# Kernel optimization log

Hardware: AMD Instinct MI355X
Metric: run time of the kernel (lower is better)

Reference implementation:

```python
import jax, jax.numpy as jnp
import numpy as np

N0_SRC, N0_DST, E0 = 495616, 45056, 450560
N1_DST, E1 = 4096, 40960
IN_FEATS, N_HIDDEN, N_CLASSES = 256, 128, 16


def setup_inputs() -> dict:
    key = jax.random.key(0)
    ks = jax.random.split(key, 12)
    x = jax.random.normal(ks[0], (N0_SRC, IN_FEATS), dtype=jnp.float32)
    src0 = jax.random.randint(ks[1], (E0,), 0, N0_SRC, dtype=jnp.int32)
    dst0 = jax.random.randint(ks[2], (E0,), 0, N0_DST, dtype=jnp.int32)
    w0 = jax.random.uniform(ks[3], (E0,), dtype=jnp.float32)
    src1 = jax.random.randint(ks[4], (E1,), 0, N0_DST, dtype=jnp.int32)
    dst1 = jax.random.randint(ks[5], (E1,), 0, N1_DST, dtype=jnp.int32)
    w1 = jax.random.uniform(ks[6], (E1,), dtype=jnp.float32)
    # xavier-uniform-ish init for linear weights
    def xavier(k, shape):
        fan_out, fan_in = shape
        lim = jnp.sqrt(6.0 / (fan_in + fan_out))
        return jax.random.uniform(k, shape, jnp.float32, -lim, lim)
    return {
        "x": x, "src0": src0, "dst0": dst0, "w0": w0,
        "src1": src1, "dst1": dst1, "w1": w1,
        "Wn0": xavier(ks[7], (N_HIDDEN, IN_FEATS)), "bn0": jnp.zeros((N_HIDDEN,), jnp.float32),
        "Wn1": xavier(ks[8], (N_HIDDEN, N_HIDDEN)), "bn1": jnp.zeros((N_HIDDEN,), jnp.float32),
        "Wfc": xavier(ks[9], (N_CLASSES, N_HIDDEN)), "bfc": jnp.zeros((N_CLASSES,), jnp.float32),
        "ndst0": N0_DST, "ndst1": N1_DST,
    }


def _weighted_sage_gcn(h, src, dst, w, Wn, bn, num_dst):
    """DGL-style 'gcn' SAGEConv with edge weights on a bipartite block.

    dst nodes are the prefix h[:num_dst] of the src node set.
    h_out = relu(fc_neigh((sum_e w_e*h[src_e] + h_dst) / (sum_e w_e + 1)))
    """
    h_dst = h[:num_dst]
    msg = h[src] * w[:, None]                                   # [E, D]
    agg = jax.ops.segment_sum(msg, dst, num_segments=num_dst)   # [num_dst, D]
    deg = jax.ops.segment_sum(w, dst, num_segments=num_dst)     # [num_dst]
    h_neigh = (agg + h_dst) / (deg[:, None] + 1.0)
    return jax.nn.relu(h_neigh @ Wn.T + bn)


def reference(x, src0, dst0, w0, src1, dst1, w1, Wn0, bn0, Wn1, bn1, Wfc, bfc, ndst0, ndst1):
    h = _weighted_sage_gcn(x, src0, dst0, w0, Wn0, bn0, ndst0)
    h = _weighted_sage_gcn(h, src1, dst1, w1, Wn1, bn1, ndst1)
    return h @ Wfc.T + bfc  # [ndst1, n_classes]
```

## Files before the change

kernel.cpp:

```cpp
#include <hip/hip_runtime.h>

#define N0_SRC 495616
#define N0_DST 45056
#define E0 450560
#define N1_DST 4096
#define E1 40960
#define IN_FEATS 256
#define NH 128
#define NC 16

__global__ void hist_kernel(const int* __restrict__ dst, int* __restrict__ cnt) {
    int e = blockIdx.x * blockDim.x + threadIdx.x;
    if (e < E0) atomicAdd(&cnt[dst[e]], 1);
}

__global__ void __launch_bounds__(1024) scan_kernel(int* __restrict__ cnt,
                                                    int* __restrict__ row_start) {
    __shared__ int partial[1024];
    const int CH = N0_DST / 1024;
    int t = threadIdx.x;
    int base = t * CH;
    int s = 0;
    for (int j = 0; j < CH; j++) s += cnt[base + j];
    partial[t] = s;
    __syncthreads();
    for (int off = 1; off < 1024; off <<= 1) {
        int v = (t >= off) ? partial[t - off] : 0;
        __syncthreads();
        partial[t] += v;
        __syncthreads();
    }
    int run = partial[t] - s;
    for (int j = 0; j < CH; j++) {
        int c = cnt[base + j];
        row_start[base + j] = run;
        cnt[base + j] = run;
        run += c;
    }
    if (t == 1023) row_start[N0_DST] = run;
}

__global__ void scatter_kernel(const int* __restrict__ dst, int* __restrict__ cursor,
                               int* __restrict__ perm) {
    int e = blockIdx.x * blockDim.x + threadIdx.x;
    if (e < E0) {
        int p = atomicAdd(&cursor[dst[e]], 1);
        perm[p] = e;
    }
}

__global__ void __launch_bounds__(256) agg0_kernel(const float* __restrict__ x,
    const int* __restrict__ src0, const float* __restrict__ w0,
    const int* __restrict__ perm, const int* __restrict__ row_start,
    float* __restrict__ hneigh) {
    int wv = blockIdx.x * 4 + (threadIdx.x >> 6);
    int lane = threadIdx.x & 63;
    if (wv >= N0_DST) return;
    int beg = row_start[wv], end = row_start[wv + 1];
    const float4* x4 = (const float4*)x;
    float4 acc = make_float4(0.f, 0.f, 0.f, 0.f);
    float degs = 0.f;
    int s = 0; float we = 0.f;
    if (beg < end) { int e = perm[beg]; s = src0[e]; we = w0[e]; }
    for (int i = beg; i < end; i++) {
        int s2 = 0; float we2 = 0.f;
        if (i + 1 < end) { int e2 = perm[i + 1]; s2 = src0[e2]; we2 = w0[e2]; }
        float4 v = x4[(size_t)s * 64 + lane];
        acc.x += we * v.x; acc.y += we * v.y; acc.z += we * v.z; acc.w += we * v.w;
        degs += we;
        s = s2; we = we2;
    }
    float4 xd = x4[(size_t)wv * 64 + lane];
    float inv = 1.0f / (degs + 1.0f);
    float4 r;
    r.x = (acc.x + xd.x) * inv; r.y = (acc.y + xd.y) * inv;
    r.z = (acc.z + xd.z) * inv; r.w = (acc.w + xd.w) * inv;
    ((float4*)hneigh)[(size_t)wv * 64 + lane] = r;
}

__global__ void __launch_bounds__(128) gemm0_kernel(const float* __restrict__ hneigh,
    const float* __restrict__ Wn, const float* __restrict__ bn,
    float* __restrict__ h0) {
    __shared__ float hn[8][IN_FEATS];
    int nb = blockIdx.x * 8;
    int tid = threadIdx.x;
    for (int i = tid; i < 8 * IN_FEATS; i += 128) {
        int n = i >> 8;
        int k = i & 255;
        hn[n][k] = hneigh[(size_t)(nb + n) * IN_FEATS + k];
    }
    __syncthreads();
    float acc[8];
#pragma unroll
    for (int n = 0; n < 8; n++) acc[n] = 0.f;
    const float4* wr4 = (const float4*)(Wn + (size_t)tid * IN_FEATS);
#pragma unroll 4
    for (int k4 = 0; k4 < IN_FEATS / 4; k4++) {
        float4 wv = wr4[k4];
        int k = k4 * 4;
#pragma unroll
        for (int n = 0; n < 8; n++) {
            acc[n] += hn[n][k + 0] * wv.x;
            acc[n] += hn[n][k + 1] * wv.y;
            acc[n] += hn[n][k + 2] * wv.z;
            acc[n] += hn[n][k + 3] * wv.w;
        }
    }
    float b = bn[tid];
#pragma unroll
    for (int n = 0; n < 8; n++) {
        float v = acc[n] + b;
        h0[(size_t)(nb + n) * NH + tid] = v > 0.f ? v : 0.f;
    }
}

__global__ void edge1_kernel(const float* __restrict__ h0,
                             const int* __restrict__ src, const int* __restrict__ dst,
                             const float* __restrict__ w,
                             float* __restrict__ agg, float* __restrict__ deg) {
    int t = blockIdx.x * blockDim.x + threadIdx.x;
    int e = t >> 5;
    int lane = t & 31;
    if (e >= E1) return;
    int s = src[e], d = dst[e];
    float we = w[e];
    float4 v = ((const float4*)(h0 + (size_t)s * NH))[lane];
    float* ad = agg + (size_t)d * NH + lane * 4;
    unsafeAtomicAdd(ad + 0, v.x * we);
    unsafeAtomicAdd(ad + 1, v.y * we);
    unsafeAtomicAdd(ad + 2, v.z * we);
    unsafeAtomicAdd(ad + 3, v.w * we);
    if (lane == 0) unsafeAtomicAdd(deg + d, we);
}

__global__ void __launch_bounds__(128) gemm1_kernel(const float* __restrict__ h0,
    const float* __restrict__ agg, const float* __restrict__ deg,
    const float* __restrict__ Wn, const float* __restrict__ bn,
    float* __restrict__ h1) {
    __shared__ float hn[8][NH];
    int nb = blockIdx.x * 8;
    int tid = threadIdx.x;
    for (int i = tid; i < 8 * NH; i += 128) {
        int n = i >> 7;
        int k = i & 127;
        int m = nb + n;
        float hv = agg[(size_t)m * NH + k] + h0[(size_t)m * NH + k];
        hn[n][k] = hv / (deg[m] + 1.0f);
    }
    __syncthreads();
    float acc[8];
#pragma unroll
    for (int n = 0; n < 8; n++) acc[n] = 0.f;
    const float4* wr4 = (const float4*)(Wn + (size_t)tid * NH);
#pragma unroll 4
    for (int k4 = 0; k4 < NH / 4; k4++) {
        float4 wv = wr4[k4];
        int k = k4 * 4;
#pragma unroll
        for (int n = 0; n < 8; n++) {
            acc[n] += hn[n][k + 0] * wv.x;
            acc[n] += hn[n][k + 1] * wv.y;
            acc[n] += hn[n][k + 2] * wv.z;
            acc[n] += hn[n][k + 3] * wv.w;
        }
    }
    float b = bn[tid];
#pragma unroll
    for (int n = 0; n < 8; n++) {
        float v = acc[n] + b;
        h1[(size_t)(nb + n) * NH + tid] = v > 0.f ? v : 0.f;
    }
}

__global__ void fc_kernel(const float* __restrict__ h1, const float* __restrict__ Wfc,
                          const float* __restrict__ bfc, float* __restrict__ out) {
    int t = blockIdx.x * blockDim.x + threadIdx.x;
    int m = t >> 4, c = t & 15;
    if (m >= N1_DST) return;
    const float* hr = h1 + (size_t)m * NH;
    const float* wr = Wfc + (size_t)c * NH;
    float acc = 0.f;
    for (int k = 0; k < NH; k++) acc += hr[k] * wr[k];
    out[t] = acc + bfc[c];
}

extern "C" void kernel_launch(void* const* d_in, const int* in_sizes, int n_in,
                              void* d_out, int out_size, void* d_ws, size_t ws_size,
                              hipStream_t stream) {
    const float* x   = (const float*)d_in[0];
    const int* src0  = (const int*)d_in[1];
    const int* dst0  = (const int*)d_in[2];
    const float* w0  = (const float*)d_in[3];
    const int* src1  = (const int*)d_in[4];
    const int* dst1  = (const int*)d_in[5];
    const float* w1  = (const float*)d_in[6];
    const float* Wn0 = (const float*)d_in[7];
    const float* bn0 = (const float*)d_in[8];
    const float* Wn1 = (const float*)d_in[9];
    const float* bn1 = (const float*)d_in[10];
    const float* Wfc = (const float*)d_in[11];
    const float* bfc = (const float*)d_in[12];
    float* out = (float*)d_out;

    float* ws = (float*)d_ws;
    float* agg1      = ws;
    float* deg1      = agg1 + (size_t)N1_DST * NH;
    int*   cnt       = (int*)(deg1 + N1_DST);
    int*   row_start = cnt + N0_DST;
    int*   perm      = row_start + N0_DST + 1;
    float* hneigh    = (float*)(perm + E0);
    float* h0        = hneigh + (size_t)N0_DST * IN_FEATS;
    float* h1        = (float*)cnt;

    size_t zero_floats = (size_t)N1_DST * NH + N1_DST + N0_DST;
    hipMemsetAsync(d_ws, 0, zero_floats * sizeof(float), stream);

    hist_kernel<<<(E0 + 255) / 256, 256, 0, stream>>>(dst0, cnt);
    scan_kernel<<<1, 1024, 0, stream>>>(cnt, row_start);
    scatter_kernel<<<(E0 + 255) / 256, 256, 0, stream>>>(dst0, cnt, perm);

    agg0_kernel<<<(N0_DST + 3) / 4, 256, 0, stream>>>(x, src0, w0, perm, row_start, hneigh);
    gemm0_kernel<<<N0_DST / 8, 128, 0, stream>>>(hneigh, Wn0, bn0, h0);

    edge1_kernel<<<(E1 * 32) / 256, 256, 0, stream>>>(h0, src1, dst1, w1, agg1, deg1);
    gemm1_kernel<<<N1_DST / 8, 128, 0, stream>>>(h0, agg1, deg1, Wn1, bn1, h1);

    fc_kernel<<<(N1_DST * NC) / 256, 256, 0, stream>>>(h1, Wfc, bfc, out);
}
```

Measured before the change: 953.7 us.

## Pack src/weight pairs in CSR scatter, unroll gather by four, widen gemm0 tile

The scatter step now writes packed (src, weight) int2 pairs in destination order, replacing the edge-id permutation. The aggregation kernel no longer needs two dependent indirect loads per edge. That kernel now issues four row gathers per iteration to keep more memory requests in flight, and gemm0 handles 16 nodes per block with vectorised LDS staging to reuse each weight load more. The workspace layout is rearranged with hard-coded offsets and the packed buffer aliases h0, which is fragile, and the larger tile raises register and LDS use.

Result: faster. 905.9 us (-5.0%).

```diff
diff --git a/kernel.cpp b/kernel.cpp
--- a/kernel.cpp
+++ b/kernel.cpp
@@ -40,66 +40,80 @@
     if (t == 1023) row_start[N0_DST] = run;
 }
 
-__global__ void scatter_kernel(const int* __restrict__ dst, int* __restrict__ cursor,
-                               int* __restrict__ perm) {
+__global__ void scatter_kernel(const int* __restrict__ dst, const int* __restrict__ src,
+                               const float* __restrict__ w, int* __restrict__ cursor,
+                               int2* __restrict__ sw) {
     int e = blockIdx.x * blockDim.x + threadIdx.x;
     if (e < E0) {
         int p = atomicAdd(&cursor[dst[e]], 1);
-        perm[p] = e;
+        sw[p] = make_int2(src[e], __float_as_int(w[e]));
     }
 }
 
 __global__ void __launch_bounds__(256) agg0_kernel(const float* __restrict__ x,
-    const int* __restrict__ src0, const float* __restrict__ w0,
-    const int* __restrict__ perm, const int* __restrict__ row_start,
+    const int2* __restrict__ sw, const int* __restrict__ row_start,
     float* __restrict__ hneigh) {
     int wv = blockIdx.x * 4 + (threadIdx.x >> 6);
     int lane = threadIdx.x & 63;
     if (wv >= N0_DST) return;
     int beg = row_start[wv], end = row_start[wv + 1];
     const float4* x4 = (const float4*)x;
-    float4 acc = make_float4(0.f, 0.f, 0.f, 0.f);
-    float degs = 0.f;
-    int s = 0; float we = 0.f;
-    if (beg < end) { int e = perm[beg]; s = src0[e]; we = w0[e]; }
-    for (int i = beg; i < end; i++) {
-        int s2 = 0; float we2 = 0.f;
-        if (i + 1 < end) { int e2 = perm[i + 1]; s2 = src0[e2]; we2 = w0[e2]; }
-        float4 v = x4[(size_t)s * 64 + lane];
-        acc.x += we * v.x; acc.y += we * v.y; acc.z += we * v.z; acc.w += we * v.w;
-        degs += we;
-        s = s2; we = we2;
-    }
     float4 xd = x4[(size_t)wv * 64 + lane];
+    float ax = 0.f, ay = 0.f, az = 0.f, aw = 0.f, degs = 0.f;
+    for (int i = beg; i < end; i += 4) {
+        int last = end - 1;
+        int i1 = (i + 1 < end) ? i + 1 : last;
+        int i2 = (i + 2 < end) ? i + 2 : last;
+        int i3 = (i + 3 < end) ? i + 3 : last;
+        int2 p0 = sw[i];
+        int2 p1 = sw[i1];
+        int2 p2 = sw[i2];
+        int2 p3 = sw[i3];
+        float4 v0 = x4[(size_t)p0.x * 64 + lane];
+        float4 v1 = x4[(size_t)p1.x * 64 + lane];
+        float4 v2 = x4[(size_t)p2.x * 64 + lane];
+        float4 v3 = x4[(size_t)p3.x * 64 + lane];
+        float w0 = __int_as_float(p0.y);
+        float w1 = (i + 1 < end) ? __int_as_float(p1.y) : 0.f;
+        float w2 = (i + 2 < end) ? __int_as_float(p2.y) : 0.f;
+        float w3 = (i + 3 < end) ? __int_as_float(p3.y) : 0.f;
+        ax = fmaf(w0, v0.x, ax); ay = fmaf(w0, v0.y, ay);
+        az = fmaf(w0, v0.z, az); aw = fmaf(w0, v0.w, aw);
+        ax = fmaf(w1, v1.x, ax); ay = fmaf(w1, v1.y, ay);
+        az = fmaf(w1, v1.z, az); aw = fmaf(w1, v1.w, aw);
+        ax = fmaf(w2, v2.x, ax); ay = fmaf(w2, v2.y, ay);
+        az = fmaf(w2, v2.z, az); aw = fmaf(w2, v2.w, aw);
+        ax = fmaf(w3, v3.x, ax); ay = fmaf(w3, v3.y, ay);
+        az = fmaf(w3, v3.z, az); aw = fmaf(w3, v3.w, aw);
+        degs += w0 + w1 + w2 + w3;
+    }
     float inv = 1.0f / (degs + 1.0f);
     float4 r;
-    r.x = (acc.x + xd.x) * inv; r.y = (acc.y + xd.y) * inv;
-    r.z = (acc.z + xd.z) * inv; r.w = (acc.w + xd.w) * inv;
+    r.x = (ax + xd.x) * inv; r.y = (ay + xd.y) * inv;
+    r.z = (az + xd.z) * inv; r.w = (aw + xd.w) * inv;
     ((float4*)hneigh)[(size_t)wv * 64 + lane] = r;
 }
 
 __global__ void __launch_bounds__(128) gemm0_kernel(const float* __restrict__ hneigh,
     const float* __restrict__ Wn, const float* __restrict__ bn,
     float* __restrict__ h0) {
-    __shared__ float hn[8][IN_FEATS];
-    int nb = blockIdx.x * 8;
+    __shared__ float hn[16][IN_FEATS];
+    int nb = blockIdx.x * 16;
     int tid = threadIdx.x;
-    for (int i = tid; i < 8 * IN_FEATS; i += 128) {
-        int n = i >> 8;
-        int k = i & 255;
-        hn[n][k] = hneigh[(size_t)(nb + n) * IN_FEATS + k];
-    }
+    const float4* s4 = (const float4*)(hneigh + (size_t)nb * IN_FEATS);
+    float4* l4 = (float4*)&hn[0][0];
+    for (int i = tid; i < 16 * IN_FEATS / 4; i += 128) l4[i] = s4[i];
     __syncthreads();
-    float acc[8];
-#pragma unroll
-    for (int n = 0; n < 8; n++) acc[n] = 0.f;
+    float acc[16];
+#pragma unroll
+    for (int n = 0; n < 16; n++) acc[n] = 0.f;
     const float4* wr4 = (const float4*)(Wn + (size_t)tid * IN_FEATS);
 #pragma unroll 4
     for (int k4 = 0; k4 < IN_FEATS / 4; k4++) {
         float4 wv = wr4[k4];
         int k = k4 * 4;
 #pragma unroll
-        for (int n = 0; n < 8; n++) {
+        for (int n = 0; n < 16; n++) {
             acc[n] += hn[n][k + 0] * wv.x;
             acc[n] += hn[n][k + 1] * wv.y;
             acc[n] += hn[n][k + 2] * wv.z;
@@ -108,7 +122,7 @@
     }
     float b = bn[tid];
 #pragma unroll
-    for (int n = 0; n < 8; n++) {
+    for (int n = 0; n < 16; n++) {
         float v = acc[n] + b;
         h0[(size_t)(nb + n) * NH + tid] = v > 0.f ? v : 0.f;
     }
@@ -207,20 +221,20 @@
     float* deg1      = agg1 + (size_t)N1_DST * NH;
     int*   cnt       = (int*)(deg1 + N1_DST);
     int*   row_start = cnt + N0_DST;
-    int*   perm      = row_start + N0_DST + 1;
-    float* hneigh    = (float*)(perm + E0);
-    float* h0        = hneigh + (size_t)N0_DST * IN_FEATS;
-    float* h1        = (float*)cnt;
+    float* hneigh    = ws + 618500;
+    float* h0        = ws + 12152836;
+    int2*  sw        = (int2*)h0;
+    float* h1        = hneigh;
 
     size_t zero_floats = (size_t)N1_DST * NH + N1_DST + N0_DST;
     hipMemsetAsync(d_ws, 0, zero_floats * sizeof(float), stream);
 
     hist_kernel<<<(E0 + 255) / 256, 256, 0, stream>>>(dst0, cnt);
     scan_kernel<<<1, 1024, 0, stream>>>(cnt, row_start);
-    scatter_kernel<<<(E0 + 255) / 256, 256, 0, stream>>>(dst0, cnt, perm);
-
-    agg0_kernel<<<(N0_DST + 3) / 4, 256, 0, stream>>>(x, src0, w0, perm, row_start, hneigh);
-    gemm0_kernel<<<N0_DST / 8, 128, 0, stream>>>(hneigh, Wn0, bn0, h0);
+    scatter_kernel<<<(E0 + 255) / 256, 256, 0, stream>>>(dst0, src0, w0, cnt, sw);
+
+    agg0_kernel<<<(N0_DST + 3) / 4, 256, 0, stream>>>(x, sw, row_start, hneigh);
+    gemm0_kernel<<<N0_DST / 16, 128, 0, stream>>>(hneigh, Wn0, bn0, h0);
 
     edge1_kernel<<<(E1 * 32) / 256, 256, 0, stream>>>(h0, src1, dst1, w1, agg1, deg1);
     gemm1_kernel<<<N1_DST / 8, 128, 0, stream>>>(h0, agg1, deg1, Wn1, bn1, h1);
```
